# Kernel tuning notes

Measured on AMD Instinct MI355X. Metric: run time of the kernel, lower is better.

## Reference

```python
import jax, jax.numpy as jnp
import numpy as np

N, E, D = 50000, 1600000, 64


def setup_inputs() -> dict:
    key = jax.random.key(0)
    ks = jax.random.split(key, 10)
    s = 1.0 / np.sqrt(D)
    return {
        "x": jax.random.normal(ks[0], (N, D), dtype=jnp.float32),
        "edge_index": jax.random.randint(ks[1], (2, E), 0, N, dtype=jnp.int64),
        "edge_weight": jax.random.uniform(ks[2], (E,), dtype=jnp.float32),
        "W_rel1": jax.random.uniform(ks[3], (D, D), jnp.float32, -s, s),
        "b_rel1": jax.random.uniform(ks[4], (D,), jnp.float32, -s, s),
        "W_root1": jax.random.uniform(ks[5], (D, D), jnp.float32, -s, s),
        "W_rel2": jax.random.uniform(ks[6], (D, D), jnp.float32, -s, s),
        "b_rel2": jax.random.uniform(ks[7], (D,), jnp.float32, -s, s),
        "W_root2": jax.random.uniform(ks[8], (D, D), jnp.float32, -s, s),
    }


def graph_conv(x, src, dst, edge_weight, W_rel, b_rel, W_root):
    # message: edge_weight * x[src]; aggregate: sum into dst
    msg = edge_weight[:, None] * x[src]                      # [E, D]
    agg = jax.ops.segment_sum(msg, dst, num_segments=x.shape[0])  # [N, D]
    return agg @ W_rel.T + b_rel + x @ W_root.T


def reference(x, edge_index, edge_weight, W_rel1, b_rel1, W_root1, W_rel2, b_rel2, W_root2):
    src, dst = edge_index[0], edge_index[1]
    h = jax.nn.relu(graph_conv(x, src, dst, edge_weight, W_rel1, b_rel1, W_root1))
    # dropout is identity in eval mode
    h = jax.nn.relu(graph_conv(h, src, dst, edge_weight, W_rel2, b_rel2, W_root2))
    return h
```

## Files before the change

### kernel.cpp

```cpp
#include <hip/hip_runtime.h>


#define NN 50000
#define DD 64
#define EE 1600000
#define NPB 64
#define NB  ((NN + NPB - 1) / NPB)
#define PAD 2560
#define CHUNK 8192
#define NC ((EE + CHUNK - 1) / CHUNK)

static_assert(NC <= 256, "colscan_kernel scan width must cover all chunks");
static_assert(NB <= 1024, "LDS cursor arrays sized for NB");

typedef __attribute__((ext_vector_type(8))) short short8;
typedef __attribute__((ext_vector_type(4))) float f32x4;

__device__ __forceinline__ unsigned short f2bf(float f) {
    unsigned u = __float_as_uint(f);
    u += 0x7FFF + ((u >> 16) & 1);
    return (unsigned short)(u >> 16);
}
__device__ __forceinline__ float bflo(unsigned u) {
    return __uint_as_float(u << 16);
}
__device__ __forceinline__ float bfhi(unsigned u) {
    return __uint_as_float(u & 0xFFFF0000u);
}
__device__ __forceinline__ unsigned char f2fp8(float f) {
    unsigned p = __builtin_amdgcn_cvt_pk_fp8_f32(f, f, 0, false);
    return (unsigned char)(p & 0xFF);
}

#define XS_STR 72
#define WS_STR 72

template <typename TIn>
__device__ __forceinline__ void transform_body(
    int blk, int t,
    const TIn* __restrict__ xin,
    const float* __restrict__ Wrel, const float* __restrict__ Wroot,
    const float* __restrict__ bias,
    unsigned char* __restrict__ Z8, unsigned short* __restrict__ Yb,
    unsigned short* Xs, unsigned short* Ws)
{
    const int node0 = blk * 64;

#pragma unroll
    for (int i = 0; i < 8; ++i) {
        int flat = i * 256 + t;
        int row  = flat >> 4;
        int c4   = flat & 15;
        const float* src = (row < 64 ? Wrel + row * 64
                                     : Wroot + (row - 64) * 64) + c4 * 4;
        float4 v = *(const float4*)src;
        unsigned short* d = &Ws[row * WS_STR + c4 * 4];
        d[0] = f2bf(v.x); d[1] = f2bf(v.y); d[2] = f2bf(v.z); d[3] = f2bf(v.w);
    }
    if constexpr (sizeof(TIn) == 4) {
#pragma unroll
        for (int i = 0; i < 4; ++i) {
            int flat = i * 256 + t;
            int row  = flat >> 4;
            int c4   = flat & 15;
            int node = node0 + row;
            float4 v = make_float4(0.f, 0.f, 0.f, 0.f);
            if (node < NN) v = *(const float4*)((const float*)xin + (size_t)node * 64 + c4 * 4);
            unsigned short* d = &Xs[row * XS_STR + c4 * 4];
            d[0] = f2bf(v.x); d[1] = f2bf(v.y); d[2] = f2bf(v.z); d[3] = f2bf(v.w);
        }
    } else {
#pragma unroll
        for (int i = 0; i < 2; ++i) {
            int flat = i * 256 + t;
            int row  = flat >> 3;
            int c8   = flat & 7;
            int node = node0 + row;
            short8 v = {0,0,0,0,0,0,0,0};
            if (node < NN)
                v = *(const short8*)((const unsigned short*)xin + (size_t)node * 64 + c8 * 8);
            *(short8*)&Xs[row * XS_STR + c8 * 8] = v;
        }
    }
    __syncthreads();

    const int w    = t >> 6;
    const int lane = t & 63;
    const int l15  = lane & 15;
    const int quad = lane >> 4;

    short8 a0 = *(const short8*)&Xs[(w * 16 + l15) * XS_STR + quad * 8];
    short8 a1 = *(const short8*)&Xs[(w * 16 + l15) * XS_STR + 32 + quad * 8];

#pragma unroll
    for (int f = 0; f < 8; ++f) {
        short8 b0 = *(const short8*)&Ws[(f * 16 + l15) * WS_STR + quad * 8];
        short8 b1 = *(const short8*)&Ws[(f * 16 + l15) * WS_STR + 32 + quad * 8];
        f32x4 acc = {0.f, 0.f, 0.f, 0.f};
        acc = __builtin_amdgcn_mfma_f32_16x16x32_bf16(a0, b0, acc, 0, 0, 0);
        acc = __builtin_amdgcn_mfma_f32_16x16x32_bf16(a1, b1, acc, 0, 0, 0);
        const int col = f * 16 + l15;
#pragma unroll
        for (int r = 0; r < 4; ++r) {
            int node = node0 + w * 16 + quad * 4 + r;
            if (node < NN) {
                if (col < 64) Z8[(size_t)node * 64 + col] = f2fp8(acc[r]);
                else          Yb[(size_t)node * 64 + (col - 64)] =
                                  f2bf(acc[r] + bias[col - 64]);
            }
        }
    }
}

__global__ __launch_bounds__(256) void hist_t1_kernel(
    const int* __restrict__ ei, int* __restrict__ hist,
    const float* __restrict__ x,
    const float* __restrict__ Wrel, const float* __restrict__ Wroot,
    const float* __restrict__ bias,
    unsigned char* __restrict__ Z8, unsigned short* __restrict__ Yb)
{
    __shared__ int lh[NB];
    __shared__ unsigned short Xs[64 * XS_STR];
    __shared__ unsigned short Ws[128 * WS_STR];
    const int t = threadIdx.x;

    if (blockIdx.x < NC) {
        const int c = blockIdx.x;
        for (int b = t; b < NB; b += 256) lh[b] = 0;
        __syncthreads();
        const int base = c * CHUNK;
#pragma unroll 4
        for (int i = 0; i < CHUNK; i += 256) {
            int e = base + i + t;
            if (e < EE) atomicAdd(&lh[ei[EE + e] >> 6], 1);
        }
        __syncthreads();
        for (int b = t; b < NB; b += 256) hist[c * NB + b] = lh[b];
    } else {
        transform_body<float>(blockIdx.x - NC, t, x, Wrel, Wroot, bias,
                              Z8, Yb, Xs, Ws);
    }
}

__global__ __launch_bounds__(256) void transform2_kernel(
    const unsigned short* __restrict__ xin,
    const float* __restrict__ Wrel, const float* __restrict__ Wroot,
    const float* __restrict__ bias,
    unsigned char* __restrict__ Z8, unsigned short* __restrict__ Yb)
{
    __shared__ unsigned short Xs[64 * XS_STR];
    __shared__ unsigned short Ws[128 * WS_STR];
    transform_body<unsigned short>(blockIdx.x, threadIdx.x, xin, Wrel, Wroot,
                                   bias, Z8, Yb, Xs, Ws);
}

__global__ __launch_bounds__(256) void colscan_kernel(
    const int* __restrict__ hist, int* __restrict__ offs, int* __restrict__ bsz)
{
    __shared__ int part[256];
    const int b = blockIdx.x, t = threadIdx.x;
    int h = (t < NC) ? hist[t * NB + b] : 0;
    part[t] = h;
    __syncthreads();
    for (int off = 1; off < 256; off <<= 1) {
        int v = (t >= off) ? part[t - off] : 0;
        __syncthreads();
        part[t] += v;
        __syncthreads();
    }
    if (t < NC) offs[t * NB + b] = b * PAD + (part[t] - h);
    if (t == 255) bsz[b] = part[255];
}

__global__ __launch_bounds__(256) void bin_kernel(
    const int* __restrict__ ei, const float* __restrict__ ew,
    const int* __restrict__ offs, unsigned* __restrict__ epk)
{
    __shared__ int cur[NB];
    const int c = blockIdx.x, t = threadIdx.x;
    for (int b = t; b < NB; b += 256) cur[b] = offs[c * NB + b];
    __syncthreads();
    const int base = c * CHUNK;
    for (int i = 0; i < CHUNK; i += 256) {
        int e = base + i + t;
        if (e < EE) {
            int src = ei[e];
            int dst = ei[EE + e];
            unsigned q = (unsigned)fmaf(ew[e], 1023.0f, 0.5f);
            int pos = atomicAdd(&cur[dst >> 6], 1);
            epk[pos] = (unsigned)src | ((unsigned)(dst & 63) << 16) | (q << 22);
        }
    }
}

__global__ __launch_bounds__(256) void sort_kernel(
    unsigned* __restrict__ epk, const int* __restrict__ bsz,
    int* __restrict__ beg, int* __restrict__ endo)
{
    __shared__ int      cnt[NPB];
    __shared__ int      cur[NPB];
    __shared__ unsigned stage[PAD];
    const int bk = blockIdx.x, t = threadIdx.x;
    const int base = bk * PAD;
    int sz = bsz[bk];
    if (sz > PAD) sz = PAD;

    if (t < NPB) cnt[t] = 0;
    __syncthreads();
    for (int i = t; i < sz; i += 256)
        atomicAdd(&cnt[(epk[base + i] >> 16) & 63], 1);
    __syncthreads();

    if (t < 64) {
        int c = cnt[t];
        int v = c;
        for (int off = 1; off < 64; off <<= 1) {
            int u = __shfl_up(v, off);
            if (t >= off) v += u;
        }
        int ex = v - c;
        cur[t] = ex;
        int g = bk * NPB + t;
        if (g < NN) { beg[g] = base + ex; endo[g] = base + ex + c; }
    }
    __syncthreads();

    for (int i = t; i < sz; i += 256) {
        unsigned p = epk[base + i];
        int pos = atomicAdd(&cur[(p >> 16) & 63], 1);
        float w = (float)(p >> 22) * (1.0f / 1023.0f);
        stage[pos] = (p & 0xFFFFu) | ((unsigned)f2bf(w) << 16);
    }
    __syncthreads();
    for (int i = t; i < sz; i += 256)
        epk[base + i] = stage[i];
}

template <bool FP32OUT>
__global__ __launch_bounds__(256) void aggregate_kernel(
    const unsigned* __restrict__ Z1,
    const uint2* __restrict__ Y4,
    const int* __restrict__ beg, const int* __restrict__ endo,
    const unsigned* __restrict__ epk, void* __restrict__ Hout)
{
    const int lane = threadIdx.x & 63;
    const int node = blockIdx.x * 4 + (threadIdx.x >> 6);
    if (node >= NN) return;
    const int s = lane & 15;
    const int q = lane >> 4;

    const int b = beg[node];
    const int e = endo[node];
    const uint2 y4 = Y4[node * 16 + s];

    float a0 = 0.f, a1 = 0.f, a2 = 0.f, a3 = 0.f;
    int i = b;
    for (; i + 16 <= e; i += 16) {
        unsigned pA = epk[i + q];
        unsigned pB = epk[i + 4 + q];
        unsigned pC = epk[i + 8 + q];
        unsigned pD = epk[i + 12 + q];
        unsigned zA = Z1[(pA & 0xFFFF) * 16 + s];
        unsigned zB = Z1[(pB & 0xFFFF) * 16 + s];
        unsigned zC = Z1[(pC & 0xFFFF) * 16 + s];
        unsigned zD = Z1[(pD & 0xFFFF) * 16 + s];
        float wA = __uint_as_float(pA & 0xFFFF0000u);
        float wB = __uint_as_float(pB & 0xFFFF0000u);
        float wC = __uint_as_float(pC & 0xFFFF0000u);
        float wD = __uint_as_float(pD & 0xFFFF0000u);
        a0 = fmaf(wA, __builtin_amdgcn_cvt_f32_fp8(zA, 0), a0);
        a1 = fmaf(wA, __builtin_amdgcn_cvt_f32_fp8(zA, 1), a1);
        a2 = fmaf(wA, __builtin_amdgcn_cvt_f32_fp8(zA, 2), a2);
        a3 = fmaf(wA, __builtin_amdgcn_cvt_f32_fp8(zA, 3), a3);
        a0 = fmaf(wB, __builtin_amdgcn_cvt_f32_fp8(zB, 0), a0);
        a1 = fmaf(wB, __builtin_amdgcn_cvt_f32_fp8(zB, 1), a1);
        a2 = fmaf(wB, __builtin_amdgcn_cvt_f32_fp8(zB, 2), a2);
        a3 = fmaf(wB, __builtin_amdgcn_cvt_f32_fp8(zB, 3), a3);
        a0 = fmaf(wC, __builtin_amdgcn_cvt_f32_fp8(zC, 0), a0);
        a1 = fmaf(wC, __builtin_amdgcn_cvt_f32_fp8(zC, 1), a1);
        a2 = fmaf(wC, __builtin_amdgcn_cvt_f32_fp8(zC, 2), a2);
        a3 = fmaf(wC, __builtin_amdgcn_cvt_f32_fp8(zC, 3), a3);
        a0 = fmaf(wD, __builtin_amdgcn_cvt_f32_fp8(zD, 0), a0);
        a1 = fmaf(wD, __builtin_amdgcn_cvt_f32_fp8(zD, 1), a1);
        a2 = fmaf(wD, __builtin_amdgcn_cvt_f32_fp8(zD, 2), a2);
        a3 = fmaf(wD, __builtin_amdgcn_cvt_f32_fp8(zD, 3), a3);
    }
    for (; i < e; i += 4) {
        int ee = i + q;
        unsigned p = (ee < e) ? epk[ee] : 0u;
        unsigned z = Z1[(p & 0xFFFF) * 16 + s];
        float w = __uint_as_float(p & 0xFFFF0000u);
        a0 = fmaf(w, __builtin_amdgcn_cvt_f32_fp8(z, 0), a0);
        a1 = fmaf(w, __builtin_amdgcn_cvt_f32_fp8(z, 1), a1);
        a2 = fmaf(w, __builtin_amdgcn_cvt_f32_fp8(z, 2), a2);
        a3 = fmaf(w, __builtin_amdgcn_cvt_f32_fp8(z, 3), a3);
    }

    a0 += __shfl_xor(a0, 16); a0 += __shfl_xor(a0, 32);
    a1 += __shfl_xor(a1, 16); a1 += __shfl_xor(a1, 32);
    a2 += __shfl_xor(a2, 16); a2 += __shfl_xor(a2, 32);
    a3 += __shfl_xor(a3, 16); a3 += __shfl_xor(a3, 32);

    if (q == 0) {
        float r0 = fmaxf(a0 + bflo(y4.x), 0.0f);
        float r1 = fmaxf(a1 + bfhi(y4.x), 0.0f);
        float r2 = fmaxf(a2 + bflo(y4.y), 0.0f);
        float r3 = fmaxf(a3 + bfhi(y4.y), 0.0f);
        if (FP32OUT) {
            ((float4*)Hout)[node * 16 + s] = make_float4(r0, r1, r2, r3);
        } else {
            uint2 o;
            o.x = (unsigned)f2bf(r0) | ((unsigned)f2bf(r1) << 16);
            o.y = (unsigned)f2bf(r2) | ((unsigned)f2bf(r3) << 16);
            ((uint2*)Hout)[node * 16 + s] = o;
        }
    }
}

extern "C" void kernel_launch(void* const* d_in, const int* in_sizes, int n_in,
                              void* d_out, int out_size, void* d_ws, size_t ws_size,
                              hipStream_t stream)
{
    const float* x     = (const float*)d_in[0];
    const int*   ei    = (const int*)  d_in[1];
    const float* ew    = (const float*)d_in[2];
    const float* Wrel1 = (const float*)d_in[3];
    const float* brel1 = (const float*)d_in[4];
    const float* Wroot1= (const float*)d_in[5];
    const float* Wrel2 = (const float*)d_in[6];
    const float* brel2 = (const float*)d_in[7];
    const float* Wroot2= (const float*)d_in[8];

    float* out = (float*)d_out;

    const size_t ND = (size_t)NN * DD;
    char* w = (char*)d_ws;
    unsigned char*  Z8 = (unsigned char*)w;
    unsigned short* Yb = (unsigned short*)(w + ND);
    unsigned short* Hb = (unsigned short*)(w + ND * 3);
    unsigned* epk = (unsigned*)(w + ND * 5);
    int* beg  = (int*)(w + ND * 5 + (size_t)NB * PAD * 4);
    int* endo = beg + NN;
    int* bsz  = endo + NN;
    int* hist = bsz + NB;
    int* offs = hist + (size_t)NC * NB;

    const int tb = (NN + 63) / 64;
    const int ab = (NN + 3) / 4;

    hist_t1_kernel<<<NC + tb, 256, 0, stream>>>(ei, hist, x, Wrel1, Wroot1,
                                                brel1, Z8, Yb);
    colscan_kernel<<<NB, 256, 0, stream>>>(hist, offs, bsz);
    bin_kernel    <<<NC, 256, 0, stream>>>(ei, ew, offs, epk);
    sort_kernel   <<<NB, 256, 0, stream>>>(epk, bsz, beg, endo);

    aggregate_kernel<false><<<ab, 256, 0, stream>>>(
        (const unsigned*)Z8, (const uint2*)Yb, beg, endo, epk, Hb);

    transform2_kernel<<<tb, 256, 0, stream>>>(Hb, Wrel2, Wroot2, brel2, Z8, Yb);
    aggregate_kernel<true><<<ab, 256, 0, stream>>>(
        (const unsigned*)Z8, (const uint2*)Yb, beg, endo, epk, out);
}
```

Baseline: 197.3 us.

## Replace bucketed two-pass binning with per-node global-atomic counting sort CSR build

Replaces the LDS-local bucket histogram, column scan, bucket binning and in-bucket sort with a direct per-node counting sort. Degrees are counted with global atomics, a two-level scan turns them into per-node offsets, and each edge is scattered with a global atomic cursor. This removes the sort pass and the padded buckets, and stores the edge weight as bf16 directly instead of a 10-bit quantised value. The cost is heavy global atomic contention spread over 50k addresses, an extra zero-init launch, and an edge order within each node that is no longer deterministic.

New measurement: 345.5 us. +75.2%, slower.

```diff
diff --git a/kernel.cpp b/kernel.cpp
--- a/kernel.cpp
+++ b/kernel.cpp
@@ -4,14 +4,12 @@
 #define NN 50000
 #define DD 64
 #define EE 1600000
-#define NPB 64
-#define NB  ((NN + NPB - 1) / NPB)
-#define PAD 2560
 #define CHUNK 8192
 #define NC ((EE + CHUNK - 1) / CHUNK)
-
-static_assert(NC <= 256, "colscan_kernel scan width must cover all chunks");
-static_assert(NB <= 1024, "LDS cursor arrays sized for NB");
+#define NSB ((NN + 255) / 256)
+
+static_assert(NSB <= 256, "scan_c scan width must cover all scan blocks");
+static_assert(EE % 256 == 0, "bin grid is exact one-edge-per-thread");
 
 typedef __attribute__((ext_vector_type(8))) short short8;
 typedef __attribute__((ext_vector_type(4))) float f32x4;
@@ -112,54 +110,58 @@
     }
 }
 
+__global__ __launch_bounds__(256) void zero_kernel(int* __restrict__ cnt)
+{
+    int i = blockIdx.x * 256 + threadIdx.x;
+    if (i < NN) cnt[i] = 0;
+}
+
 __global__ __launch_bounds__(256) void hist_t1_kernel(
-    const int* __restrict__ ei, int* __restrict__ hist,
+    const int* __restrict__ ei, int* __restrict__ cnt,
     const float* __restrict__ x,
     const float* __restrict__ Wrel, const float* __restrict__ Wroot,
     const float* __restrict__ bias,
     unsigned char* __restrict__ Z8, unsigned short* __restrict__ Yb)
 {
-    __shared__ int lh[NB];
     __shared__ unsigned short Xs[64 * XS_STR];
     __shared__ unsigned short Ws[128 * WS_STR];
     const int t = threadIdx.x;
 
     if (blockIdx.x < NC) {
-        const int c = blockIdx.x;
-        for (int b = t; b < NB; b += 256) lh[b] = 0;
-        __syncthreads();
-        const int base = c * CHUNK;
+        const int base = blockIdx.x * CHUNK;
 #pragma unroll 4
         for (int i = 0; i < CHUNK; i += 256) {
             int e = base + i + t;
-            if (e < EE) atomicAdd(&lh[ei[EE + e] >> 6], 1);
-        }
-        __syncthreads();
-        for (int b = t; b < NB; b += 256) hist[c * NB + b] = lh[b];
+            if (e < EE) atomicAdd(&cnt[ei[EE + e]], 1);
+        }
     } else {
         transform_body<float>(blockIdx.x - NC, t, x, Wrel, Wroot, bias,
                               Z8, Yb, Xs, Ws);
     }
 }
 
-__global__ __launch_bounds__(256) void transform2_kernel(
-    const unsigned short* __restrict__ xin,
-    const float* __restrict__ Wrel, const float* __restrict__ Wroot,
-    const float* __restrict__ bias,
-    unsigned char* __restrict__ Z8, unsigned short* __restrict__ Yb)
-{
-    __shared__ unsigned short Xs[64 * XS_STR];
-    __shared__ unsigned short Ws[128 * WS_STR];
-    transform_body<unsigned short>(blockIdx.x, threadIdx.x, xin, Wrel, Wroot,
-                                   bias, Z8, Yb, Xs, Ws);
-}
-
-__global__ __launch_bounds__(256) void colscan_kernel(
-    const int* __restrict__ hist, int* __restrict__ offs, int* __restrict__ bsz)
+__global__ __launch_bounds__(256) void scan_a(
+    const int* __restrict__ cnt, int* __restrict__ btot)
+{
+    __shared__ int wsum[4];
+    const int b = blockIdx.x, t = threadIdx.x;
+    int n = b * 256 + t;
+    int v = (n < NN) ? cnt[n] : 0;
+    for (int off = 1; off < 64; off <<= 1) v += __shfl_xor(v, off);
+    if ((t & 63) == 0) wsum[t >> 6] = v;
+    __syncthreads();
+    if (t == 0) btot[b] = wsum[0] + wsum[1] + wsum[2] + wsum[3];
+}
+
+__global__ __launch_bounds__(256) void scan_c(
+    const int* __restrict__ cnt, const int* __restrict__ btot,
+    int* __restrict__ beg, int* __restrict__ endo, int* __restrict__ cur)
 {
     __shared__ int part[256];
+    __shared__ int nods[256];
     const int b = blockIdx.x, t = threadIdx.x;
-    int h = (t < NC) ? hist[t * NB + b] : 0;
+
+    int h = (t < NSB) ? btot[t] : 0;
     part[t] = h;
     __syncthreads();
     for (int off = 1; off < 256; off <<= 1) {
@@ -168,72 +170,36 @@
         part[t] += v;
         __syncthreads();
     }
-    if (t < NC) offs[t * NB + b] = b * PAD + (part[t] - h);
-    if (t == 255) bsz[b] = part[255];
+    const int P = part[b] - btot[b];
+
+    const int n = b * 256 + t;
+    const int c = (n < NN) ? cnt[n] : 0;
+    nods[t] = c;
+    __syncthreads();
+    for (int off = 1; off < 256; off <<= 1) {
+        int v = (t >= off) ? nods[t - off] : 0;
+        __syncthreads();
+        nods[t] += v;
+        __syncthreads();
+    }
+    if (n < NN) {
+        int bg = P + nods[t] - c;
+        beg[n]  = bg;
+        endo[n] = bg + c;
+        cur[n]  = bg;
+    }
 }
 
 __global__ __launch_bounds__(256) void bin_kernel(
     const int* __restrict__ ei, const float* __restrict__ ew,
-    const int* __restrict__ offs, unsigned* __restrict__ epk)
-{
-    __shared__ int cur[NB];
-    const int c = blockIdx.x, t = threadIdx.x;
-    for (int b = t; b < NB; b += 256) cur[b] = offs[c * NB + b];
-    __syncthreads();
-    const int base = c * CHUNK;
-    for (int i = 0; i < CHUNK; i += 256) {
-        int e = base + i + t;
-        if (e < EE) {
-            int src = ei[e];
-            int dst = ei[EE + e];
-            unsigned q = (unsigned)fmaf(ew[e], 1023.0f, 0.5f);
-            int pos = atomicAdd(&cur[dst >> 6], 1);
-            epk[pos] = (unsigned)src | ((unsigned)(dst & 63) << 16) | (q << 22);
-        }
-    }
-}
-
-__global__ __launch_bounds__(256) void sort_kernel(
-    unsigned* __restrict__ epk, const int* __restrict__ bsz,
-    int* __restrict__ beg, int* __restrict__ endo)
-{
-    __shared__ int      cnt[NPB];
-    __shared__ int      cur[NPB];
-    __shared__ unsigned stage[PAD];
-    const int bk = blockIdx.x, t = threadIdx.x;
-    const int base = bk * PAD;
-    int sz = bsz[bk];
-    if (sz > PAD) sz = PAD;
-
-    if (t < NPB) cnt[t] = 0;
-    __syncthreads();
-    for (int i = t; i < sz; i += 256)
-        atomicAdd(&cnt[(epk[base + i] >> 16) & 63], 1);
-    __syncthreads();
-
-    if (t < 64) {
-        int c = cnt[t];
-        int v = c;
-        for (int off = 1; off < 64; off <<= 1) {
-            int u = __shfl_up(v, off);
-            if (t >= off) v += u;
-        }
-        int ex = v - c;
-        cur[t] = ex;
-        int g = bk * NPB + t;
-        if (g < NN) { beg[g] = base + ex; endo[g] = base + ex + c; }
-    }
-    __syncthreads();
-
-    for (int i = t; i < sz; i += 256) {
-        unsigned p = epk[base + i];
-        int pos = atomicAdd(&cur[(p >> 16) & 63], 1);
-        float w = (float)(p >> 22) * (1.0f / 1023.0f);
-        stage[pos] = (p & 0xFFFFu) | ((unsigned)f2bf(w) << 16);
-    }
-    __syncthreads();
-    for (int i = t; i < sz; i += 256)
-        epk[base + i] = stage[i];
+    int* __restrict__ cur, unsigned* __restrict__ epk)
+{
+    const int e = blockIdx.x * 256 + threadIdx.x;
+    int src = ei[e];
+    int dst = ei[EE + e];
+    unsigned w = f2bf(ew[e]);
+    int pos = atomicAdd(&cur[dst], 1);
+    epk[pos] = (unsigned)src | (w << 16);
 }
 
 template <bool FP32OUT>
@@ -317,6 +283,18 @@
     }
 }
 
+__global__ __launch_bounds__(256) void transform2_kernel(
+    const unsigned short* __restrict__ xin,
+    const float* __restrict__ Wrel, const float* __restrict__ Wroot,
+    const float* __restrict__ bias,
+    unsigned char* __restrict__ Z8, unsigned short* __restrict__ Yb)
+{
+    __shared__ unsigned short Xs[64 * XS_STR];
+    __shared__ unsigned short Ws[128 * WS_STR];
+    transform_body<unsigned short>(blockIdx.x, threadIdx.x, xin, Wrel, Wroot,
+                                   bias, Z8, Yb, Xs, Ws);
+}
+
 extern "C" void kernel_launch(void* const* d_in, const int* in_sizes, int n_in,
                               void* d_out, int out_size, void* d_ws, size_t ws_size,
                               hipStream_t stream)
@@ -339,20 +317,21 @@
     unsigned short* Yb = (unsigned short*)(w + ND);
     unsigned short* Hb = (unsigned short*)(w + ND * 3);
     unsigned* epk = (unsigned*)(w + ND * 5);
-    int* beg  = (int*)(w + ND * 5 + (size_t)NB * PAD * 4);
+    int* cnt  = (int*)(w + ND * 5 + (size_t)EE * 4);
+    int* beg  = cnt + NN;
     int* endo = beg + NN;
-    int* bsz  = endo + NN;
-    int* hist = bsz + NB;
-    int* offs = hist + (size_t)NC * NB;
+    int* cur  = endo + NN;
+    int* btot = cur + NN;
 
     const int tb = (NN + 63) / 64;
     const int ab = (NN + 3) / 4;
 
-    hist_t1_kernel<<<NC + tb, 256, 0, stream>>>(ei, hist, x, Wrel1, Wroot1,
+    zero_kernel<<<NSB, 256, 0, stream>>>(cnt);
+    hist_t1_kernel<<<NC + tb, 256, 0, stream>>>(ei, cnt, x, Wrel1, Wroot1,
                                                 brel1, Z8, Yb);
-    colscan_kernel<<<NB, 256, 0, stream>>>(hist, offs, bsz);
-    bin_kernel    <<<NC, 256, 0, stream>>>(ei, ew, offs, epk);
-    sort_kernel   <<<NB, 256, 0, stream>>>(epk, bsz, beg, endo);
+    scan_a<<<NSB, 256, 0, stream>>>(cnt, btot);
+    scan_c<<<NSB, 256, 0, stream>>>(cnt, btot, beg, endo, cur);
+    bin_kernel<<<EE / 256, 256, 0, stream>>>(ei, ew, cur, epk);
 
     aggregate_kernel<false><<<ab, 256, 0, stream>>>(
         (const unsigned*)Z8, (const uint2*)Yb, beg, endo, epk, Hb);
```

## Fuse per-bucket edge sort into aggregate kernel using LDS-staged edges

Applied to the files above, without the earlier changes.

The separate sort kernel is removed. Each aggregate block now loads its destination bucket, counting-sorts the edges into shared memory, and aggregates 64 nodes from LDS, with 8 waves each handling 8 nodes. This drops one launch, the global beg/endo arrays and the global write-back of the sorted edges. In exchange the sort is repeated in both aggregate passes, and the grid shrinks to one 512-thread block per 64 nodes, which reduces the number of waves available to hide gather latency.

Result: no change. 199.0 us (+0.9%).

```diff
diff --git a/kernel.cpp b/kernel.cpp
--- a/kernel.cpp
+++ b/kernel.cpp
@@ -151,7 +151,7 @@
     __shared__ unsigned short Xs[64 * XS_STR];
     __shared__ unsigned short Ws[128 * WS_STR];
     transform_body<unsigned short>(blockIdx.x, threadIdx.x, xin, Wrel, Wroot,
-                                   bias, Z8, Yb, Xs, Ws);
+                                   bias, Xs == nullptr ? Z8 : Z8, Yb, Xs, Ws);
 }
 
 __global__ __launch_bounds__(256) void colscan_kernel(
@@ -193,11 +193,15 @@
     }
 }
 
-__global__ __launch_bounds__(256) void sort_kernel(
-    unsigned* __restrict__ epk, const int* __restrict__ bsz,
-    int* __restrict__ beg, int* __restrict__ endo)
+template <bool FP32OUT>
+__global__ __launch_bounds__(512) void aggregate_kernel(
+    const unsigned* __restrict__ Z1,
+    const uint2* __restrict__ Y4,
+    const int* __restrict__ bsz,
+    const unsigned* __restrict__ epk, void* __restrict__ Hout)
 {
     __shared__ int      cnt[NPB];
+    __shared__ int      nbeg[NPB];
     __shared__ int      cur[NPB];
     __shared__ unsigned stage[PAD];
     const int bk = blockIdx.x, t = threadIdx.x;
@@ -207,7 +211,7 @@
 
     if (t < NPB) cnt[t] = 0;
     __syncthreads();
-    for (int i = t; i < sz; i += 256)
+    for (int i = t; i < sz; i += 512)
         atomicAdd(&cnt[(epk[base + i] >> 16) & 63], 1);
     __syncthreads();
 
@@ -218,101 +222,93 @@
             int u = __shfl_up(v, off);
             if (t >= off) v += u;
         }
-        int ex = v - c;
-        cur[t] = ex;
-        int g = bk * NPB + t;
-        if (g < NN) { beg[g] = base + ex; endo[g] = base + ex + c; }
-    }
-    __syncthreads();
-
-    for (int i = t; i < sz; i += 256) {
+        nbeg[t] = v - c;
+        cur[t]  = v - c;
+    }
+    __syncthreads();
+
+    for (int i = t; i < sz; i += 512) {
         unsigned p = epk[base + i];
         int pos = atomicAdd(&cur[(p >> 16) & 63], 1);
         float w = (float)(p >> 22) * (1.0f / 1023.0f);
         stage[pos] = (p & 0xFFFFu) | ((unsigned)f2bf(w) << 16);
     }
     __syncthreads();
-    for (int i = t; i < sz; i += 256)
-        epk[base + i] = stage[i];
-}
-
-template <bool FP32OUT>
-__global__ __launch_bounds__(256) void aggregate_kernel(
-    const unsigned* __restrict__ Z1,
-    const uint2* __restrict__ Y4,
-    const int* __restrict__ beg, const int* __restrict__ endo,
-    const unsigned* __restrict__ epk, void* __restrict__ Hout)
-{
-    const int lane = threadIdx.x & 63;
-    const int node = blockIdx.x * 4 + (threadIdx.x >> 6);
-    if (node >= NN) return;
+
+    const int lane = t & 63;
+    const int wv   = t >> 6;
     const int s = lane & 15;
     const int q = lane >> 4;
 
-    const int b = beg[node];
-    const int e = endo[node];
-    const uint2 y4 = Y4[node * 16 + s];
-
-    float a0 = 0.f, a1 = 0.f, a2 = 0.f, a3 = 0.f;
-    int i = b;
-    for (; i + 16 <= e; i += 16) {
-        unsigned pA = epk[i + q];
-        unsigned pB = epk[i + 4 + q];
-        unsigned pC = epk[i + 8 + q];
-        unsigned pD = epk[i + 12 + q];
-        unsigned zA = Z1[(pA & 0xFFFF) * 16 + s];
-        unsigned zB = Z1[(pB & 0xFFFF) * 16 + s];
-        unsigned zC = Z1[(pC & 0xFFFF) * 16 + s];
-        unsigned zD = Z1[(pD & 0xFFFF) * 16 + s];
-        float wA = __uint_as_float(pA & 0xFFFF0000u);
-        float wB = __uint_as_float(pB & 0xFFFF0000u);
-        float wC = __uint_as_float(pC & 0xFFFF0000u);
-        float wD = __uint_as_float(pD & 0xFFFF0000u);
-        a0 = fmaf(wA, __builtin_amdgcn_cvt_f32_fp8(zA, 0), a0);
-        a1 = fmaf(wA, __builtin_amdgcn_cvt_f32_fp8(zA, 1), a1);
-        a2 = fmaf(wA, __builtin_amdgcn_cvt_f32_fp8(zA, 2), a2);
-        a3 = fmaf(wA, __builtin_amdgcn_cvt_f32_fp8(zA, 3), a3);
-        a0 = fmaf(wB, __builtin_amdgcn_cvt_f32_fp8(zB, 0), a0);
-        a1 = fmaf(wB, __builtin_amdgcn_cvt_f32_fp8(zB, 1), a1);
-        a2 = fmaf(wB, __builtin_amdgcn_cvt_f32_fp8(zB, 2), a2);
-        a3 = fmaf(wB, __builtin_amdgcn_cvt_f32_fp8(zB, 3), a3);
-        a0 = fmaf(wC, __builtin_amdgcn_cvt_f32_fp8(zC, 0), a0);
-        a1 = fmaf(wC, __builtin_amdgcn_cvt_f32_fp8(zC, 1), a1);
-        a2 = fmaf(wC, __builtin_amdgcn_cvt_f32_fp8(zC, 2), a2);
-        a3 = fmaf(wC, __builtin_amdgcn_cvt_f32_fp8(zC, 3), a3);
-        a0 = fmaf(wD, __builtin_amdgcn_cvt_f32_fp8(zD, 0), a0);
-        a1 = fmaf(wD, __builtin_amdgcn_cvt_f32_fp8(zD, 1), a1);
-        a2 = fmaf(wD, __builtin_amdgcn_cvt_f32_fp8(zD, 2), a2);
-        a3 = fmaf(wD, __builtin_amdgcn_cvt_f32_fp8(zD, 3), a3);
-    }
-    for (; i < e; i += 4) {
-        int ee = i + q;
-        unsigned p = (ee < e) ? epk[ee] : 0u;
-        unsigned z = Z1[(p & 0xFFFF) * 16 + s];
-        float w = __uint_as_float(p & 0xFFFF0000u);
-        a0 = fmaf(w, __builtin_amdgcn_cvt_f32_fp8(z, 0), a0);
-        a1 = fmaf(w, __builtin_amdgcn_cvt_f32_fp8(z, 1), a1);
-        a2 = fmaf(w, __builtin_amdgcn_cvt_f32_fp8(z, 2), a2);
-        a3 = fmaf(w, __builtin_amdgcn_cvt_f32_fp8(z, 3), a3);
-    }
-
-    a0 += __shfl_xor(a0, 16); a0 += __shfl_xor(a0, 32);
-    a1 += __shfl_xor(a1, 16); a1 += __shfl_xor(a1, 32);
-    a2 += __shfl_xor(a2, 16); a2 += __shfl_xor(a2, 32);
-    a3 += __shfl_xor(a3, 16); a3 += __shfl_xor(a3, 32);
-
-    if (q == 0) {
-        float r0 = fmaxf(a0 + bflo(y4.x), 0.0f);
-        float r1 = fmaxf(a1 + bfhi(y4.x), 0.0f);
-        float r2 = fmaxf(a2 + bflo(y4.y), 0.0f);
-        float r3 = fmaxf(a3 + bfhi(y4.y), 0.0f);
-        if (FP32OUT) {
-            ((float4*)Hout)[node * 16 + s] = make_float4(r0, r1, r2, r3);
-        } else {
-            uint2 o;
-            o.x = (unsigned)f2bf(r0) | ((unsigned)f2bf(r1) << 16);
-            o.y = (unsigned)f2bf(r2) | ((unsigned)f2bf(r3) << 16);
-            ((uint2*)Hout)[node * 16 + s] = o;
+#pragma unroll
+    for (int k = 0; k < 8; ++k) {
+        const int n6   = wv * 8 + k;
+        const int node = bk * 64 + n6;
+        const int b = nbeg[n6];
+        const int e = b + cnt[n6];
+
+        float a0 = 0.f, a1 = 0.f, a2 = 0.f, a3 = 0.f;
+        int i = b;
+        for (; i + 16 <= e; i += 16) {
+            unsigned pA = stage[i + q];
+            unsigned pB = stage[i + 4 + q];
+            unsigned pC = stage[i + 8 + q];
+            unsigned pD = stage[i + 12 + q];
+            unsigned zA = Z1[(pA & 0xFFFF) * 16 + s];
+            unsigned zB = Z1[(pB & 0xFFFF) * 16 + s];
+            unsigned zC = Z1[(pC & 0xFFFF) * 16 + s];
+            unsigned zD = Z1[(pD & 0xFFFF) * 16 + s];
+            float wA = __uint_as_float(pA & 0xFFFF0000u);
+            float wB = __uint_as_float(pB & 0xFFFF0000u);
+            float wC = __uint_as_float(pC & 0xFFFF0000u);
+            float wD = __uint_as_float(pD & 0xFFFF0000u);
+            a0 = fmaf(wA, __builtin_amdgcn_cvt_f32_fp8(zA, 0), a0);
+            a1 = fmaf(wA, __builtin_amdgcn_cvt_f32_fp8(zA, 1), a1);
+            a2 = fmaf(wA, __builtin_amdgcn_cvt_f32_fp8(zA, 2), a2);
+            a3 = fmaf(wA, __builtin_amdgcn_cvt_f32_fp8(zA, 3), a3);
+            a0 = fmaf(wB, __builtin_amdgcn_cvt_f32_fp8(zB, 0), a0);
+            a1 = fmaf(wB, __builtin_amdgcn_cvt_f32_fp8(zB, 1), a1);
+            a2 = fmaf(wB, __builtin_amdgcn_cvt_f32_fp8(zB, 2), a2);
+            a3 = fmaf(wB, __builtin_amdgcn_cvt_f32_fp8(zB, 3), a3);
+            a0 = fmaf(wC, __builtin_amdgcn_cvt_f32_fp8(zC, 0), a0);
+            a1 = fmaf(wC, __builtin_amdgcn_cvt_f32_fp8(zC, 1), a1);
+            a2 = fmaf(wC, __builtin_amdgcn_cvt_f32_fp8(zC, 2), a2);
+            a3 = fmaf(wC, __builtin_amdgcn_cvt_f32_fp8(zC, 3), a3);
+            a0 = fmaf(wD, __builtin_amdgcn_cvt_f32_fp8(zD, 0), a0);
+            a1 = fmaf(wD, __builtin_amdgcn_cvt_f32_fp8(zD, 1), a1);
+            a2 = fmaf(wD, __builtin_amdgcn_cvt_f32_fp8(zD, 2), a2);
+            a3 = fmaf(wD, __builtin_amdgcn_cvt_f32_fp8(zD, 3), a3);
+        }
+        for (; i < e; i += 4) {
+            int ee = i + q;
+            unsigned p = (ee < e) ? stage[ee] : 0u;
+            unsigned z = Z1[(p & 0xFFFF) * 16 + s];
+            float w = __uint_as_float(p & 0xFFFF0000u);
+            a0 = fmaf(w, __builtin_amdgcn_cvt_f32_fp8(z, 0), a0);
+            a1 = fmaf(w, __builtin_amdgcn_cvt_f32_fp8(z, 1), a1);
+            a2 = fmaf(w, __builtin_amdgcn_cvt_f32_fp8(z, 2), a2);
+            a3 = fmaf(w, __builtin_amdgcn_cvt_f32_fp8(z, 3), a3);
+        }
+
+        a0 += __shfl_xor(a0, 16); a0 += __shfl_xor(a0, 32);
+        a1 += __shfl_xor(a1, 16); a1 += __shfl_xor(a1, 32);
+        a2 += __shfl_xor(a2, 16); a2 += __shfl_xor(a2, 32);
+        a3 += __shfl_xor(a3, 16); a3 += __shfl_xor(a3, 32);
+
+        if (q == 0 && node < NN) {
+            const uint2 y4 = Y4[node * 16 + s];
+            float r0 = fmaxf(a0 + bflo(y4.x), 0.0f);
+            float r1 = fmaxf(a1 + bfhi(y4.x), 0.0f);
+            float r2 = fmaxf(a2 + bflo(y4.y), 0.0f);
+            float r3 = fmaxf(a3 + bfhi(y4.y), 0.0f);
+            if (FP32OUT) {
+                ((float4*)Hout)[node * 16 + s] = make_float4(r0, r1, r2, r3);
+            } else {
+                uint2 o;
+                o.x = (unsigned)f2bf(r0) | ((unsigned)f2bf(r1) << 16);
+                o.y = (unsigned)f2bf(r2) | ((unsigned)f2bf(r3) << 16);
+                ((uint2*)Hout)[node * 16 + s] = o;
+            }
         }
     }
 }
@@ -339,25 +335,21 @@
     unsigned short* Yb = (unsigned short*)(w + ND);
     unsigned short* Hb = (unsigned short*)(w + ND * 3);
     unsigned* epk = (unsigned*)(w + ND * 5);
-    int* beg  = (int*)(w + ND * 5 + (size_t)NB * PAD * 4);
-    int* endo = beg + NN;
-    int* bsz  = endo + NN;
+    int* bsz  = (int*)(w + ND * 5 + (size_t)NB * PAD * 4);
     int* hist = bsz + NB;
     int* offs = hist + (size_t)NC * NB;
 
     const int tb = (NN + 63) / 64;
-    const int ab = (NN + 3) / 4;
 
     hist_t1_kernel<<<NC + tb, 256, 0, stream>>>(ei, hist, x, Wrel1, Wroot1,
                                                 brel1, Z8, Yb);
     colscan_kernel<<<NB, 256, 0, stream>>>(hist, offs, bsz);
     bin_kernel    <<<NC, 256, 0, stream>>>(ei, ew, offs, epk);
-    sort_kernel   <<<NB, 256, 0, stream>>>(epk, bsz, beg, endo);
-
-    aggregate_kernel<false><<<ab, 256, 0, stream>>>(
-        (const unsigned*)Z8, (const uint2*)Yb, beg, endo, epk, Hb);
+
+    aggregate_kernel<false><<<NB, 512, 0, stream>>>(
+        (const unsigned*)Z8, (const uint2*)Yb, bsz, epk, Hb);
 
     transform2_kernel<<<tb, 256, 0, stream>>>(Hb, Wrel2, Wroot2, brel2, Z8, Yb);
-    aggregate_kernel<true><<<ab, 256, 0, stream>>>(
-        (const unsigned*)Z8, (const uint2*)Yb, beg, endo, epk, out);
-}
+    aggregate_kernel<true><<<NB, 512, 0, stream>>>(
+        (const unsigned*)Z8, (const uint2*)Yb, bsz, epk, out);
+}
```
